# Kernel tuning notes

Hardware: AMD Instinct MI355X
Metric: run time of the kernel (lower is better)

Reference implementation:

```python
import jax, jax.numpy as jnp
import numpy as np

Z, Y, X = 16, 128, 128
B = 2
N_R, N_L = 12000, 20000   # active voxels per batch element (radar / lidar)
C = 64
IN_DIM = 4
NUM_LAYER = 2
K_LIST = (64, 32)         # knn fan-out = 64 / 2**layer
EPS = 1e-5


def _make_voxels(rng, n_per_batch):
    # unique voxel coords per batch, sorted by linear index (batch-major rows)
    out = []
    for b in range(B):
        lin = np.sort(rng.choice(Z * Y * X, size=n_per_batch, replace=False))
        z = lin // (Y * X); y = (lin // X) % Y; x = lin % X
        out.append(np.stack([np.full(n_per_batch, b), z, y, x], 1))
    return np.concatenate(out, 0).astype(np.int32)


def _nbr_map(coords):
    # 3x3x3 submanifold-conv rulebook: row index of each neighbor, -1 if absent
    b = coords[:, 0].astype(np.int64); z = coords[:, 1]; y = coords[:, 2]; x = coords[:, 3]
    keys = ((b * Z + z) * Y + y) * X + x  # globally sorted
    N = coords.shape[0]
    nbr = np.full((N, 27), -1, np.int64)
    k = 0
    for dz in (-1, 0, 1):
        for dy in (-1, 0, 1):
            for dx in (-1, 0, 1):
                nz, ny, nx = z + dz, y + dy, x + dx
                ok = (nz >= 0) & (nz < Z) & (ny >= 0) & (ny < Y) & (nx >= 0) & (nx < X)
                cand = ((b * Z + nz) * Y + ny) * X + nx
                pos = np.searchsorted(keys, cand)
                pos_c = np.clip(pos, 0, N - 1)
                hit = ok & (keys[pos_c] == cand)
                nbr[:, k] = np.where(hit, pos_c, -1)
                k += 1
    return nbr


def setup_inputs() -> dict:
    rng = np.random.default_rng(0)
    key = jax.random.key(0)
    ks = jax.random.split(key, 16)
    coordsR = _make_voxels(rng, N_R)
    coordsL = _make_voxels(rng, N_L)
    nbrR = _nbr_map(coordsR)
    nbrL = _nbr_map(coordsL)
    NLt = B * N_L
    # knn indices (global row ids into radar rows of same batch)
    knn0 = coordsL[:, 0:1].astype(np.int64) * N_R + rng.integers(0, N_R, (NLt, K_LIST[0]))
    knn1 = coordsL[:, 0:1].astype(np.int64) * N_R + rng.integers(0, N_R, (NLt, K_LIST[1]))
    sc = 1.0 / np.sqrt(27 * C).astype(np.float32)
    inp = {
        "featR": jax.random.normal(ks[0], (B * N_R, IN_DIM), jnp.float32),
        "featL": jax.random.normal(ks[1], (NLt, IN_DIM), jnp.float32),
        "img": jax.random.normal(ks[2], (B, 512), jnp.float32),
        "Win": jax.random.normal(ks[3], (2, IN_DIM, C), jnp.float32) * 0.1,
        "bin_": jnp.zeros((2, C), jnp.float32),
        # [layer, branch(R/L), conv(sp,subm_a,subm_b), 27, Cin, Cout]
        "Wconv": jax.random.normal(ks[4], (NUM_LAYER, 2, 3, 27, C, C), jnp.float32) * sc,
        "bconv": jnp.zeros((NUM_LAYER, 2, 3, C), jnp.float32),
        "bng": jnp.ones((NUM_LAYER, 2, 3, C), jnp.float32),
        "bnb": jnp.zeros((NUM_LAYER, 2, 3, C), jnp.float32),
        "Wimg": jax.random.normal(ks[5], (NUM_LAYER, 512, C), jnp.float32) * 0.05,
        "bimg": jnp.zeros((NUM_LAYER, C), jnp.float32),
        "Wval": jax.random.normal(ks[6], (NUM_LAYER, C, C), jnp.float32) * 0.125,
        "bval": jnp.zeros((NUM_LAYER, C), jnp.float32),
        "Wgate": jax.random.normal(ks[7], (NUM_LAYER, 2 * C, C), jnp.float32) * 0.09,
        "bgate": jnp.zeros((NUM_LAYER, C), jnp.float32),
        "Wbev": jax.random.normal(ks[8], (NUM_LAYER, 2, C * Z, C, 3, 3), jnp.float32) * (1.0 / np.sqrt(C * Z * 9).astype(np.float32)),
        "bbev": jnp.zeros((NUM_LAYER, 2, C), jnp.float32),
        "bntg": jnp.ones((NUM_LAYER, 2, C), jnp.float32),
        "bntb": jnp.zeros((NUM_LAYER, 2, C), jnp.float32),
        "nbrR": jnp.asarray(nbrR),
        "nbrL": jnp.asarray(nbrL),
        "knn0": jnp.asarray(knn0),
        "knn1": jnp.asarray(knn1),
        "coordsR": jnp.asarray(coordsR),
        "coordsL": jnp.asarray(coordsL),
    }
    return inp


def _bn1d(f, g, b):
    m = f.mean(0)
    v = f.var(0)
    return (f - m) / jnp.sqrt(v + EPS) * g + b


def _sconv(f, nbr, W, bias):
    # gather-scatter sparse 3D conv: out[n] = sum_k W[k] @ f[nbr[n,k]]
    mask = (nbr >= 0)[..., None].astype(f.dtype)
    g = f[jnp.clip(nbr, 0)] * mask                 # [N, 27, C]
    return jnp.einsum('nkc,kcd->nd', g, W) + bias


def _branch_block(f, nbr, Wc, bc, g, bt):
    # spconv -> bn -> relu, subm_a -> bn -> relu, subm_b -> bn -> relu
    for j in range(3):
        f = jax.nn.relu(_bn1d(_sconv(f, nbr, Wc[j], bc[j]), g[j], bt[j]))
    return f


def _to_bev(f, coords, Wt, bt, gg, gb):
    dense = jnp.zeros((B, Z, Y, X, C), f.dtype).at[
        coords[:, 0], coords[:, 1], coords[:, 2], coords[:, 3]].add(f)
    x2 = dense.transpose(0, 4, 1, 2, 3).reshape(B, C * Z, Y, X)  # 'b c z y x -> b (c z) y x'
    # ConvTranspose2d(k=3, s=1, p=1) == conv with swapped-IO, spatially flipped kernel, pad 1
    Wk = jnp.transpose(Wt, (1, 0, 2, 3))[:, :, ::-1, ::-1]
    out = jax.lax.conv_general_dilated(x2, Wk, (1, 1), ((1, 1), (1, 1)),
                                       dimension_numbers=('NCHW', 'OIHW', 'NCHW'))
    out = out + bt[:, None, None]
    m = out.mean((0, 2, 3), keepdims=True)
    v = out.var((0, 2, 3), keepdims=True)
    out = (out - m) / jnp.sqrt(v + EPS) * gg[:, None, None] + gb[:, None, None]
    return jax.nn.relu(out)


def reference(featR, featL, img, Win, bin_, Wconv, bconv, bng, bnb, Wimg, bimg,
              Wval, bval, Wgate, bgate, Wbev, bbev, bntg, bntb,
              nbrR, nbrL, knn0, knn1, coordsR, coordsL):
    fR = featR @ Win[0] + bin_[0]   # input_convR (1x1x1)
    fL = featL @ Win[1] + bin_[1]   # input_convL (1x1x1)
    knns = (knn0, knn1)
    bidL = coordsL[:, 0]
    bevs = []
    for l in range(NUM_LAYER):
        fR = _branch_block(fR, nbrR, Wconv[l, 0], bconv[l, 0], bng[l, 0], bnb[l, 0])
        fL = _branch_block(fL, nbrL, Wconv[l, 1], bconv[l, 1], bng[l, 1], bnb[l, 1])
        # knn cross-attention fusion: lidar queries K nearest radar voxels
        key = fR[knns[l]]                                        # [NL, K, C]
        val = jnp.einsum('nkc,cd->nkd', key, Wval[l]) + bval[l]
        attn = jax.nn.softmax(jnp.einsum('nc,nkc->nk', fL, key), axis=-1)
        fused = jnp.einsum('nk,nkd->nd', attn, val)
        imgf = jax.nn.sigmoid(img @ Wimg[l] + bimg[l])           # [B, C] weather condition
        fused = fused * imgf[bidL]
        gate = jax.nn.sigmoid(jnp.concatenate([fL, fused], -1) @ Wgate[l] + bgate[l])
        fL = fL + gate * fused
        bevs.append(_to_bev(fR, coordsR, Wbev[l, 0], bbev[l, 0], bntg[l, 0], bntb[l, 0]))
        bevs.append(_to_bev(fL, coordsL, Wbev[l, 1], bbev[l, 1], bntg[l, 1], bntb[l, 1]))
    return jnp.concatenate(bevs, axis=1)  # [B, 4*C, Y, X]
```

## Files before the change

### kernel.cpp

```cpp
#include <hip/hip_runtime.h>
#include <math.h>

#define NRT 24000
#define NLT 40000

static __device__ __forceinline__ float sigmoidf_(float x){ return 1.0f/(1.0f+expf(-x)); }

static __device__ __forceinline__ int xcd_swz(int bid, int nwg){
  int q = nwg>>3, r = nwg&7, x = bid&7, i = bid>>3;
  return (x<r ? x*(q+1) : r*(q+1)+(x-r)*q) + i;
}

__global__ void k_proj(const float* __restrict__ feat, const float* __restrict__ W,
                       const float* __restrict__ bias, float* __restrict__ out, int N){
  int i = blockIdx.x*256 + threadIdx.x;
  if (i >= N*64) return;
  int n = i >> 6, c = i & 63;
  const float* f = feat + n*4;
  out[i] = fmaf(f[0], W[c], fmaf(f[1], W[64+c], fmaf(f[2], W[128+c], fmaf(f[3], W[192+c], bias[c]))));
}

__global__ void k_kmask16(const int* __restrict__ nbr, int NG, int* __restrict__ kmask){
  int g = blockIdx.x*64 + threadIdx.x;
  if (g >= NG) return;
  int m = 0;
  for (int v=0;v<16;v++){
    const int* row = nbr + (size_t)(g*16+v)*27;
    for (int k=0;k<27;k++) if (row[k] >= 0) m |= (1<<k);
  }
  kmask[g] = m;
}

__global__ void k_wc(const float* __restrict__ Wconv, float* __restrict__ WcT){
  int i = blockIdx.x*256+threadIdx.x;
  if (i >= 12*27*16*64*4) return;
  int j = i & 3; int r = i >> 2;
  int d = r & 63; r >>= 6;
  int c4 = r & 15; r >>= 4;
  int k = r % 27; int lc = r / 27;
  WcT[i] = Wconv[(size_t)lc*110592 + (size_t)k*4096 + (size_t)(4*c4+j)*64 + d];
}

__global__ void k_sconv(const float* __restrict__ fin, const int* __restrict__ nbr,
                        const int* __restrict__ kmask, const float* __restrict__ W,
                        float* __restrict__ psum, size_t pstride, int N){
  int t = threadIdx.x & 63;
  int sub = threadIdx.x >> 6;
  int g = xcd_swz(blockIdx.x, gridDim.x);
  int n0 = g*16;
  float acc[16];
  #pragma unroll
  for (int v=0;v<16;v++) acc[v] = 0.f;
  const int* nrow = nbr + (size_t)n0*27;
  int m = kmask[g] & (0x7F << (7*sub));
  while (m){
    int k = __builtin_ctz(m); m &= m-1;
    const float4* w4 = reinterpret_cast<const float4*>(W) + k*1024 + t;
    float4 wreg[16];
    #pragma unroll
    for (int c4=0;c4<16;c4++) wreg[c4] = w4[c4*64];
    #pragma unroll
    for (int v=0;v<16;v++){
      int nb = nrow[27*v + k];
      if (nb >= 0){
        const float4* fr = reinterpret_cast<const float4*>(fin + (size_t)nb*64);
        float4 a = make_float4(0.f,0.f,0.f,0.f);
        #pragma unroll
        for (int c4=0;c4<16;c4++){
          float4 fv = fr[c4];
          a.x = fmaf(fv.x, wreg[c4].x, a.x);
          a.y = fmaf(fv.y, wreg[c4].y, a.y);
          a.z = fmaf(fv.z, wreg[c4].z, a.z);
          a.w = fmaf(fv.w, wreg[c4].w, a.w);
        }
        acc[v] += (a.x+a.y)+(a.z+a.w);
      }
    }
  }
  float* po = psum + (size_t)sub*pstride;
  #pragma unroll
  for (int v=0;v<16;v++) po[(size_t)(n0+v)*64 + t] = acc[v];
}

__global__ void k_colsum4(const float* __restrict__ p, size_t st, int N,
                          float* __restrict__ partial){
  int d = threadIdx.x & 63, sub = threadIdx.x >> 6;
  float s=0.f, s2=0.f;
  for (int n = blockIdx.x*4 + sub; n < N; n += 1024){
    size_t i = (size_t)n*64+d;
    float v = p[i] + p[i+st] + p[i+2*st] + p[i+3*st];
    s += v; s2 = fmaf(v,v,s2);
  }
  __shared__ float ls[4][64], ls2[4][64];
  ls[sub][d]=s; ls2[sub][d]=s2;
  __syncthreads();
  if (sub==0){
    s  = ls[0][d]+ls[1][d]+ls[2][d]+ls[3][d];
    s2 = ls2[0][d]+ls2[1][d]+ls2[2][d]+ls2[3][d];
    partial[(blockIdx.x*64+d)*2+0]=s;
    partial[(blockIdx.x*64+d)*2+1]=s2;
  }
}

__global__ void k_bnfin(const float* __restrict__ partial, int nblk, float invN,
                        const float* __restrict__ g, const float* __restrict__ b,
                        float* __restrict__ mv){
  int t = threadIdx.x, d = t & 63, sub = t >> 6;
  float s=0.f, s2=0.f;
  for (int i=sub;i<nblk;i+=4){ s += partial[(i*64+d)*2]; s2 += partial[(i*64+d)*2+1]; }
  __shared__ float ls[4][64], ls2[4][64];
  ls[sub][d]=s; ls2[sub][d]=s2;
  __syncthreads();
  if (sub==0){
    s  = ls[0][d]+ls[1][d]+ls[2][d]+ls[3][d];
    s2 = ls2[0][d]+ls2[1][d]+ls2[2][d]+ls2[3][d];
    float mean = s*invN;
    float var  = s2*invN - mean*mean;
    float rstd = 1.0f/sqrtf(var + 1e-5f);
    float sc = g[d]*rstd;
    mv[d*2]   = sc;
    mv[d*2+1] = b[d] - mean*sc;
  }
}

__global__ void k_bnrelu4(const float* __restrict__ p, size_t st,
                          const float* __restrict__ mv, float* __restrict__ fout, int total){
  int i = blockIdx.x*256+threadIdx.x;
  if (i>=total) return;
  int c = i & 63;
  float s = p[i] + p[i+st] + p[i+2*st] + p[i+3*st];
  float v = fmaf(s, mv[c*2], mv[c*2+1]);
  fout[i] = v>0.f? v:0.f;
}

__global__ void k_imgf(const float* __restrict__ img, const float* __restrict__ Wimg,
                       const float* __restrict__ bimg, float* __restrict__ imgf){
  int t = threadIdx.x;
  int b = t>>6, c = t&63;
  float s = bimg[c];
  const float* ir = img + b*512;
  for (int j=0;j<512;j++) s = fmaf(ir[j], Wimg[j*64+c], s);
  imgf[b*64+c] = sigmoidf_(s);
}

__global__ void k_attn(float* __restrict__ fL, const float* __restrict__ fR,
                       const int* __restrict__ knn, const int* __restrict__ coordsL,
                       const float* __restrict__ Wval, const float* __restrict__ bval,
                       const float* __restrict__ Wgate, const float* __restrict__ bgate,
                       const float* __restrict__ imgf, int K){
  __shared__ float keys[64*65];
  __shared__ float fls[64];
  __shared__ float aw[64];
  __shared__ float wks[64];
  __shared__ float fus[64];
  int n = blockIdx.x, t = threadIdx.x;
  float fl = fL[(size_t)n*64+t];
  fls[t] = fl;
  const int* kn = knn + (size_t)n*K;
  for (int k=0;k<K;k++){
    int r = kn[k];
    keys[k*65+t] = fR[(size_t)r*64+t];
  }
  __syncthreads();
  float s = -1e30f;
  if (t < K){
    const float* kr = keys + t*65;
    float a0 = 0.f;
    #pragma unroll
    for (int c=0;c<64;c++) a0 = fmaf(fls[c], kr[c], a0);
    s = a0;
  }
  float mx = s;
  #pragma unroll
  for (int m=32;m;m>>=1) mx = fmaxf(mx, __shfl_xor(mx, m, 64));
  float e = (t<K) ? expf(s-mx) : 0.f;
  float se = e;
  #pragma unroll
  for (int m=32;m;m>>=1) se += __shfl_xor(se, m, 64);
  aw[t] = e/se;
  __syncthreads();
  float wk = 0.f;
  for (int k=0;k<K;k++) wk = fmaf(aw[k], keys[k*65+t], wk);
  wks[t] = wk;
  __syncthreads();
  float fu = bval[t];
  #pragma unroll
  for (int c=0;c<64;c++) fu = fmaf(wks[c], Wval[c*64+t], fu);
  int bid = coordsL[n*4];
  fu *= imgf[bid*64+t];
  fus[t] = fu;
  __syncthreads();
  float gs = bgate[t];
  #pragma unroll
  for (int c=0;c<64;c++) gs = fmaf(fls[c], Wgate[c*64+t], gs);
  #pragma unroll
  for (int c=0;c<64;c++) gs = fmaf(fus[c], Wgate[(64+c)*64+t], gs);
  float gate = sigmoidf_(gs);
  fL[(size_t)n*64+t] = fl + gate*fu;
}

__global__ void k_grid(const int* __restrict__ coords, int N, int* __restrict__ grid){
  int n = blockIdx.x*256+threadIdx.x;
  if (n>=N) return;
  int b=coords[n*4], z=coords[n*4+1], y=coords[n*4+2], x=coords[n*4+3];
  grid[((b*128+y)*128+x)*16+z] = n;
}

__global__ void k_colbuild(const int* __restrict__ grid, int* __restrict__ ccnt,
                           int* __restrict__ cent){
  int col = blockIdx.x*256+threadIdx.x;
  if (col >= 2*128*128) return;
  const int* g = grid + col*16;
  int c=0;
  for (int z=0;z<16;z++){ int v=g[z]; if (v>=0) cent[col*16 + (c++)] = (v<<4)|z; }
  ccnt[col]=c;
}

__global__ void k_zbound(const int* __restrict__ coords, int N, int* __restrict__ zs){
  int n = blockIdx.x*256+threadIdx.x;
  if (n>=N) return;
  int key = coords[n*4]*16 + coords[n*4+1];
  int pk = (n>0) ? coords[(n-1)*4]*16 + coords[(n-1)*4+1] : -1;
  for (int kk=pk+1; kk<=key; kk++) zs[kk] = n;
  if (n==N-1){ for (int kk=key+1; kk<=32; kk++) zs[kk] = N; }
}

__global__ void k_wt3(const float* __restrict__ Wbev, float* __restrict__ Wt3){
  int i = blockIdx.x*256+threadIdx.x;
  if (i >= 4*9*16*16*64*4) return;
  int j = i & 3; int r = i >> 2;
  int o = r & 63; r >>= 6;
  int c4 = r & 15; r >>= 4;
  int z = r & 15; r >>= 4;
  int q = r % 9; int ls = r / 9;
  int c = 4*c4 + j;
  int ky = 2-q/3, kx = 2-q%3;
  Wt3[i] = Wbev[(size_t)ls*589824 + (size_t)(c*16+z)*576 + o*9 + ky*3 + kx];
}

__global__ void k_bevg(const float* __restrict__ f, const int* __restrict__ zs,
                       const float* __restrict__ Wt,
                       float* __restrict__ tmp, int CH){
  int task = blockIdx.x / CH, chunk = blockIdx.x % CH;
  int q = task >> 4, z = task & 15;
  int t = threadIdx.x;
  const float4* w4 = reinterpret_cast<const float4*>(Wt + (size_t)(((q<<4)+z)<<12)) + t;
  float4 wreg[16];
  #pragma unroll
  for (int c4=0;c4<16;c4++) wreg[c4] = w4[c4*64];
  int s0 = zs[z], c0 = zs[z+1]-s0;
  int s1 = zs[16+z], c1 = zs[17+z]-s1;
  int total = c0 + c1;
  for (int i=chunk; i<total; i+=CH){
    int v = (i<c0) ? s0+i : s1+(i-c0);
    const float4* fr = reinterpret_cast<const float4*>(f + (size_t)v*64);
    float4 a = make_float4(0.f,0.f,0.f,0.f);
    #pragma unroll
    for (int c4=0;c4<16;c4++){
      float4 fv = fr[c4];
      a.x = fmaf(fv.x, wreg[c4].x, a.x);
      a.y = fmaf(fv.y, wreg[c4].y, a.y);
      a.z = fmaf(fv.z, wreg[c4].z, a.z);
      a.w = fmaf(fv.w, wreg[c4].w, a.w);
    }
    tmp[((size_t)v*9+q)*64 + t] = (a.x+a.y)+(a.z+a.w);
  }
}

__global__ void k_bevs(const float* __restrict__ tmp, const int* __restrict__ ccnt,
                       const int* __restrict__ cent, float* __restrict__ outp){
  int blk = xcd_swz(blockIdx.x, gridDim.x);
  int b = blk>>12; int rem = blk&4095; int y = rem>>5; int x0 = (rem&31)<<2;
  int t = threadIdx.x;
  float acc[4] = {0.f,0.f,0.f,0.f};
  #pragma unroll
  for (int dy=-1;dy<=1;dy++){
    int y2 = y+dy;
    if ((unsigned)y2 >= 128u) continue;
    int qb = (dy+1)*3 + 1;
    for (int cx=x0-1; cx<=x0+4; cx++){
      if ((unsigned)cx >= 128u) continue;
      int col = ((b<<7)+y2)*128 + cx;
      int cn = ccnt[col];
      const int* ce = cent + col*16;
      int d0 = cx - x0;
      for (int i=0;i<cn;i++){
        int rid = ce[i]>>4;
        const float* tb = tmp + (size_t)rid*576 + qb*64 + t;
        #pragma unroll
        for (int v=0;v<4;v++){
          int dx = d0 - v;
          if (dx>=-1 && dx<=1) acc[v] += tb[dx*64];
        }
      }
    }
  }
  float4 o4 = make_float4(acc[0],acc[1],acc[2],acc[3]);
  *reinterpret_cast<float4*>(outp + (size_t)b*(256*16384) + (size_t)t*16384 + y*128 + x0) = o4;
}

__global__ void k_bevstat(const float* __restrict__ outp, const float* __restrict__ g,
                          const float* __restrict__ b, float* __restrict__ mv){
  int ch = blockIdx.x, t = threadIdx.x;
  float s=0.f, s2=0.f;
  for (int bb=0;bb<2;bb++){
    const float* base = outp + (size_t)bb*(256*16384) + (size_t)ch*16384;
    for (int p=t;p<16384;p+=256){ float v = base[p]; s+=v; s2=fmaf(v,v,s2); }
  }
  __shared__ float ls[256], ls2[256];
  ls[t]=s; ls2[t]=s2; __syncthreads();
  for (int m=128;m;m>>=1){ if (t<m){ ls[t]+=ls[t+m]; ls2[t]+=ls2[t+m]; } __syncthreads(); }
  if (t==0){
    float mean = ls[0]*(1.0f/32768.0f);
    float var  = ls2[0]*(1.0f/32768.0f) - mean*mean;
    float rstd = 1.0f/sqrtf(var+1e-5f);
    float sc = g[ch]*rstd;
    mv[ch*2]=sc; mv[ch*2+1]=b[ch]-mean*sc;
  }
}

__global__ void k_bevbn(float* __restrict__ outp, const float* __restrict__ mv){
  int i = blockIdx.x*256+threadIdx.x;
  if (i >= 2*64*16384) return;
  int bb = i>>20; int r = i & ((1<<20)-1);
  int ch = r>>14; int p = r&16383;
  float* a = outp + (size_t)bb*(256*16384) + (size_t)ch*16384 + p;
  float v = fmaf(*a, mv[ch*2], mv[ch*2+1]);
  *a = v>0.f? v:0.f;
}

extern "C" void kernel_launch(void* const* d_in, const int* in_sizes, int n_in,
                              void* d_out, int out_size, void* d_ws, size_t ws_size,
                              hipStream_t stream){
  const float* featR = (const float*)d_in[0];
  const float* featL = (const float*)d_in[1];
  const float* img   = (const float*)d_in[2];
  const float* Win   = (const float*)d_in[3];
  const float* bin_  = (const float*)d_in[4];
  const float* Wconv = (const float*)d_in[5];
  const float* bng   = (const float*)d_in[7];
  const float* bnb   = (const float*)d_in[8];
  const float* Wimg  = (const float*)d_in[9];
  const float* bimg  = (const float*)d_in[10];
  const float* Wval  = (const float*)d_in[11];
  const float* bval  = (const float*)d_in[12];
  const float* Wgate = (const float*)d_in[13];
  const float* bgate = (const float*)d_in[14];
  const float* Wbev  = (const float*)d_in[15];
  const float* bntg  = (const float*)d_in[17];
  const float* bntb  = (const float*)d_in[18];
  const int* nbrR    = (const int*)d_in[19];
  const int* nbrL    = (const int*)d_in[20];
  const int* knn0    = (const int*)d_in[21];
  const int* knn1    = (const int*)d_in[22];
  const int* coordsR = (const int*)d_in[23];
  const int* coordsL = (const int*)d_in[24];
  float* outp = (float*)d_out;

  char* w = (char*)d_ws;
  auto alloc = [&](size_t bytes){ char* p = w; w += (bytes + 255) & ~(size_t)255; return p; };
  float* fRa = (float*)alloc((size_t)NRT*64*4);
  float* fLa = (float*)alloc((size_t)NLT*64*4);
  int*   gridR = (int*)alloc((size_t)2*128*128*16*4);
  int*   gridL = (int*)alloc((size_t)2*128*128*16*4);
  float* Wt3 = (float*)alloc((size_t)4*9*16*16*64*4*4);
  float* WcT = (float*)alloc((size_t)12*27*16*64*4*4);
  float* imgfbuf = (float*)alloc(2*64*4);
  float* partial = (float*)alloc((size_t)256*64*2*4);
  float* mv = (float*)alloc(64*2*4);
  int* kmaskR = (int*)alloc((size_t)(NRT/16)*4);
  int* kmaskL = (int*)alloc((size_t)(NLT/16)*4);
  int* ccntR = (int*)alloc((size_t)2*128*128*4);
  int* ccntL = (int*)alloc((size_t)2*128*128*4);
  int* centR = (int*)alloc((size_t)2*128*128*16*4);
  int* centL = (int*)alloc((size_t)2*128*128*16*4);
  int* zsR = (int*)alloc(33*4);
  int* zsL = (int*)alloc(33*4);
  char* big = alloc((size_t)NLT*576*4);
  float* tmp  = (float*)big;
  float* psum = (float*)big;
  const size_t PST = (size_t)NLT*64;

  hipMemsetAsync(gridR, 0xFF, (size_t)2*128*128*16*4, stream);
  hipMemsetAsync(gridL, 0xFF, (size_t)2*128*128*16*4, stream);
  k_grid<<<(NRT+255)/256,256,0,stream>>>(coordsR, NRT, gridR);
  k_grid<<<(NLT+255)/256,256,0,stream>>>(coordsL, NLT, gridL);
  k_colbuild<<<(2*128*128+255)/256,256,0,stream>>>(gridR, ccntR, centR);
  k_colbuild<<<(2*128*128+255)/256,256,0,stream>>>(gridL, ccntL, centL);
  k_zbound<<<(NRT+255)/256,256,0,stream>>>(coordsR, NRT, zsR);
  k_zbound<<<(NLT+255)/256,256,0,stream>>>(coordsL, NLT, zsL);
  k_kmask16<<<((NRT/16)+63)/64,64,0,stream>>>(nbrR, NRT/16, kmaskR);
  k_kmask16<<<((NLT/16)+63)/64,64,0,stream>>>(nbrL, NLT/16, kmaskL);
  k_wt3<<<(4*9*16*16*64*4+255)/256,256,0,stream>>>(Wbev, Wt3);
  k_wc<<<(12*27*16*64*4+255)/256,256,0,stream>>>(Wconv, WcT);

  k_proj<<<(NRT*64+255)/256,256,0,stream>>>(featR, Win,     bin_,    fRa, NRT);
  k_proj<<<(NLT*64+255)/256,256,0,stream>>>(featL, Win+256, bin_+64, fLa, NLT);

  const int CH = 32;
  for (int l=0;l<2;l++){
    for (int j=0;j<3;j++){
      const float* Wc = WcT + (size_t)((l*2+0)*3+j)*110592;
      k_sconv<<<NRT/16,256,0,stream>>>(fRa, nbrR, kmaskR, Wc, psum, PST, NRT);
      k_colsum4<<<256,256,0,stream>>>(psum, PST, NRT, partial);
      k_bnfin<<<1,256,0,stream>>>(partial, 256, 1.0f/NRT,
                                  bng + ((l*2+0)*3+j)*64, bnb + ((l*2+0)*3+j)*64, mv);
      k_bnrelu4<<<(NRT*64+255)/256,256,0,stream>>>(psum, PST, mv, fRa, NRT*64);
    }
    for (int j=0;j<3;j++){
      const float* Wc = WcT + (size_t)((l*2+1)*3+j)*110592;
      k_sconv<<<NLT/16,256,0,stream>>>(fLa, nbrL, kmaskL, Wc, psum, PST, NLT);
      k_colsum4<<<256,256,0,stream>>>(psum, PST, NLT, partial);
      k_bnfin<<<1,256,0,stream>>>(partial, 256, 1.0f/NLT,
                                  bng + ((l*2+1)*3+j)*64, bnb + ((l*2+1)*3+j)*64, mv);
      k_bnrelu4<<<(NLT*64+255)/256,256,0,stream>>>(psum, PST, mv, fLa, NLT*64);
    }
    k_imgf<<<1,128,0,stream>>>(img, Wimg + (size_t)l*512*64, bimg + l*64, imgfbuf);
    const int* knn = (l==0)? knn0 : knn1;
    int K = (l==0)? 64 : 32;
    k_attn<<<NLT,64,0,stream>>>(fLa, fRa, knn, coordsL,
                                Wval + (size_t)l*4096, bval + l*64,
                                Wgate + (size_t)l*8192, bgate + l*64,
                                imgfbuf, K);
    {
      float* op = outp + (size_t)(2*l)*64*16384;
      const float* wt = Wt3 + (size_t)(l*2+0)*589824;
      k_bevg<<<144*CH,64,0,stream>>>(fRa, zsR, wt, tmp, CH);
      k_bevs<<<2*128*32,64,0,stream>>>(tmp, ccntR, centR, op);
      k_bevstat<<<64,256,0,stream>>>(op, bntg + (l*2+0)*64, bntb + (l*2+0)*64, mv);
      k_bevbn<<<(2*64*16384+255)/256,256,0,stream>>>(op, mv);
    }
    {
      float* op = outp + (size_t)(2*l+1)*64*16384;
      const float* wt = Wt3 + (size_t)(l*2+1)*589824;
      k_bevg<<<144*CH,64,0,stream>>>(fLa, zsL, wt, tmp, CH);
      k_bevs<<<2*128*32,64,0,stream>>>(tmp, ccntL, centL, op);
      k_bevstat<<<64,256,0,stream>>>(op, bntg + (l*2+1)*64, bntb + (l*2+1)*64, mv);
      k_bevbn<<<(2*64*16384+255)/256,256,0,stream>>>(op, mv);
    }
  }
}
```

Baseline: 3.266 ms.

## Replace masked group sparse conv with offset-sorted pair list SpMM and reduction

The sparse 3x3x3 conv no longer loops over 16-voxel groups under a union kernel-offset mask, which wasted work on absent neighbours. It now builds a compacted list of (offset, voxel) pairs sorted by offset and splits it evenly across 2048 waves, reloading weights only when the offset changes. Each pair's contribution goes to a per-voxel slot in a contrib buffer, and a separate reduction kernel sums them. This removes the 4-way partial-sum buffers but adds several prep kernels, extra global traffic for contributions, and a reduce pass. The BEV gather kernel also gains XCD swizzling with a reordered task mapping.

```diff
diff --git a/kernel.cpp b/kernel.cpp
--- a/kernel.cpp
+++ b/kernel.cpp
@@ -20,15 +20,71 @@
   out[i] = fmaf(f[0], W[c], fmaf(f[1], W[64+c], fmaf(f[2], W[128+c], fmaf(f[3], W[192+c], bias[c]))));
 }
 
-__global__ void k_kmask16(const int* __restrict__ nbr, int NG, int* __restrict__ kmask){
-  int g = blockIdx.x*64 + threadIdx.x;
-  if (g >= NG) return;
-  int m = 0;
-  for (int v=0;v<16;v++){
-    const int* row = nbr + (size_t)(g*16+v)*27;
-    for (int k=0;k<27;k++) if (row[k] >= 0) m |= (1<<k);
-  }
-  kmask[g] = m;
+__global__ void k_mask(const int* __restrict__ nbr, int N, int* __restrict__ mask){
+  int n = blockIdx.x*256+threadIdx.x;
+  if (n>=N) return;
+  const int* row = nbr + (size_t)n*27;
+  int m=0;
+  #pragma unroll
+  for (int k=0;k<27;k++) if (row[k]>=0) m |= 1<<k;
+  mask[n]=m;
+}
+
+__global__ void k_wsum(const int* __restrict__ mask, int N, int* __restrict__ wsum){
+  int n = blockIdx.x*256+threadIdx.x;
+  int pc = (n<N)? __popc(mask[n]) : 0;
+  #pragma unroll
+  for (int s=32;s;s>>=1) pc += __shfl_down(pc, s, 64);
+  if ((threadIdx.x&63)==0) wsum[(blockIdx.x*256+threadIdx.x)>>6] = pc;
+}
+
+__global__ void k_scan(const int* __restrict__ in, int M, int* __restrict__ out){
+  __shared__ int buf[704];
+  for (int i=threadIdx.x;i<M;i+=256) buf[i]=in[i];
+  __syncthreads();
+  if (threadIdx.x==0){ int s=0; for (int i=0;i<M;i++){ int v=buf[i]; buf[i]=s; s+=v; } buf[M]=s; }
+  __syncthreads();
+  for (int i=threadIdx.x;i<=M;i+=256) out[i]=buf[i];
+}
+
+__global__ void k_noff(const int* __restrict__ mask, const int* __restrict__ woff,
+                       int N, int* __restrict__ noff){
+  int n = blockIdx.x*256+threadIdx.x;
+  if (n>=N) return;
+  int lane = threadIdx.x&63;
+  int pc = __popc(mask[n]);
+  int pre = pc;
+  #pragma unroll
+  for (int s=1;s<64;s<<=1){ int v=__shfl_up(pre, s, 64); if (lane>=s) pre+=v; }
+  noff[n] = woff[n>>6] + pre - pc;
+  if (n==N-1) noff[N] = woff[N>>6];
+}
+
+__global__ void k_kcnt2(const int* __restrict__ mask, int N, int* __restrict__ cnt2){
+  int k = blockIdx.x>>3, seg = blockIdx.x&7;
+  int s0 = seg*(N/8), s1 = s0 + N/8;
+  int c=0;
+  for (int n=s0+threadIdx.x;n<s1;n+=256) c += (mask[n]>>k)&1;
+  __shared__ int ls[256];
+  ls[threadIdx.x]=c; __syncthreads();
+  for (int m=128;m;m>>=1){ if (threadIdx.x<m) ls[threadIdx.x]+=ls[threadIdx.x+m]; __syncthreads(); }
+  if (threadIdx.x==0) cnt2[blockIdx.x]=ls[0];
+}
+
+__global__ void k_kfill2(const int* __restrict__ mask, int N, const int* __restrict__ off2,
+                         unsigned* __restrict__ pairs){
+  int w = (blockIdx.x*256+threadIdx.x)>>6;
+  int lane = threadIdx.x&63;
+  int k = w>>3, seg = w&7;
+  int s0 = seg*(N/8), s1 = s0 + N/8;
+  int base = off2[w];
+  for (int n0=s0;n0<s1;n0+=64){
+    int n = n0+lane;
+    int v = (n<s1) && ((mask[n]>>k)&1);
+    unsigned long long bal = __ballot(v);
+    if (v) pairs[base + (int)__popcll(bal & ((1ull<<lane)-1))] = ((unsigned)k<<16)|(unsigned)n;
+    base += (int)__popcll(bal);
+  }
 }
 
 __global__ void k_wc(const float* __restrict__ Wconv, float* __restrict__ WcT){
@@ -41,54 +97,58 @@
   WcT[i] = Wconv[(size_t)lc*110592 + (size_t)k*4096 + (size_t)(4*c4+j)*64 + d];
 }
 
-__global__ void k_sconv(const float* __restrict__ fin, const int* __restrict__ nbr,
-                        const int* __restrict__ kmask, const float* __restrict__ W,
-                        float* __restrict__ psum, size_t pstride, int N){
-  int t = threadIdx.x & 63;
-  int sub = threadIdx.x >> 6;
-  int g = xcd_swz(blockIdx.x, gridDim.x);
-  int n0 = g*16;
-  float acc[16];
-  #pragma unroll
-  for (int v=0;v<16;v++) acc[v] = 0.f;
-  const int* nrow = nbr + (size_t)n0*27;
-  int m = kmask[g] & (0x7F << (7*sub));
-  while (m){
-    int k = __builtin_ctz(m); m &= m-1;
-    const float4* w4 = reinterpret_cast<const float4*>(W) + k*1024 + t;
-    float4 wreg[16];
+__global__ void k_spmm(const float* __restrict__ fin, const int* __restrict__ nbr,
+                       const int* __restrict__ mask, const int* __restrict__ noff,
+                       const int* __restrict__ off2, const unsigned* __restrict__ pairs,
+                       const float* __restrict__ W, float* __restrict__ contrib, int nwaves){
+  int wid = (blockIdx.x*256+threadIdx.x)>>6;
+  int t = threadIdx.x&63;
+  int total = off2[216];
+  int a = (int)(((long long)wid*total)/nwaves);
+  int b = (int)(((long long)(wid+1)*total)/nwaves);
+  int kcur = -1;
+  float4 wreg[16];
+  for (int i=a;i<b;i++){
+    unsigned pk = pairs[i];
+    int k = pk>>16, n = pk&0xFFFF;
+    if (k!=kcur){
+      kcur=k;
+      const float4* w4 = reinterpret_cast<const float4*>(W) + k*1024 + t;
+      #pragma unroll
+      for (int c4=0;c4<16;c4++) wreg[c4]=w4[c4*64];
+    }
+    int nb = nbr[(size_t)n*27+k];
+    const float4* fr = reinterpret_cast<const float4*>(fin + (size_t)nb*64);
+    float4 a4 = make_float4(0.f,0.f,0.f,0.f);
     #pragma unroll
-    for (int c4=0;c4<16;c4++) wreg[c4] = w4[c4*64];
-    #pragma unroll
-    for (int v=0;v<16;v++){
-      int nb = nrow[27*v + k];
-      if (nb >= 0){
-        const float4* fr = reinterpret_cast<const float4*>(fin + (size_t)nb*64);
-        float4 a = make_float4(0.f,0.f,0.f,0.f);
-        #pragma unroll
-        for (int c4=0;c4<16;c4++){
-          float4 fv = fr[c4];
-          a.x = fmaf(fv.x, wreg[c4].x, a.x);
-          a.y = fmaf(fv.y, wreg[c4].y, a.y);
-          a.z = fmaf(fv.z, wreg[c4].z, a.z);
-          a.w = fmaf(fv.w, wreg[c4].w, a.w);
-        }
-        acc[v] += (a.x+a.y)+(a.z+a.w);
-      }
-    }
-  }
-  float* po = psum + (size_t)sub*pstride;
-  #pragma unroll
-  for (int v=0;v<16;v++) po[(size_t)(n0+v)*64 + t] = acc[v];
-}
-
-__global__ void k_colsum4(const float* __restrict__ p, size_t st, int N,
-                          float* __restrict__ partial){
+    for (int c4=0;c4<16;c4++){
+      float4 fv = fr[c4];
+      a4.x = fmaf(fv.x, wreg[c4].x, a4.x);
+      a4.y = fmaf(fv.y, wreg[c4].y, a4.y);
+      a4.z = fmaf(fv.z, wreg[c4].z, a4.z);
+      a4.w = fmaf(fv.w, wreg[c4].w, a4.w);
+    }
+    int rank = __popc(mask[n] & ((1<<k)-1));
+    contrib[((size_t)noff[n]+rank)*64 + t] = (a4.x+a4.y)+(a4.z+a4.w);
+  }
+}
+
+__global__ void k_sred(const float* __restrict__ contrib, const int* __restrict__ noff,
+                       float* __restrict__ out, int N){
+  int n = (blockIdx.x*256+threadIdx.x)>>6;
+  if (n>=N) return;
+  int t = threadIdx.x&63;
+  int j0=noff[n], j1=noff[n+1];
+  float s=0.f;
+  for (int j=j0;j<j1;j++) s += contrib[(size_t)j*64+t];
+  out[(size_t)n*64+t]=s;
+}
+
+__global__ void k_colsum(const float* __restrict__ f, int N, float* __restrict__ partial){
   int d = threadIdx.x & 63, sub = threadIdx.x >> 6;
   float s=0.f, s2=0.f;
   for (int n = blockIdx.x*4 + sub; n < N; n += 1024){
-    size_t i = (size_t)n*64+d;
-    float v = p[i] + p[i+st] + p[i+2*st] + p[i+3*st];
+    float v = f[(size_t)n*64+d];
     s += v; s2 = fmaf(v,v,s2);
   }
   __shared__ float ls[4][64], ls2[4][64];
@@ -123,13 +183,12 @@
   }
 }
 
-__global__ void k_bnrelu4(const float* __restrict__ p, size_t st,
-                          const float* __restrict__ mv, float* __restrict__ fout, int total){
+__global__ void k_bnrelu(const float* __restrict__ cv, const float* __restrict__ mv,
+                         float* __restrict__ fout, int total){
   int i = blockIdx.x*256+threadIdx.x;
   if (i>=total) return;
   int c = i & 63;
-  float s = p[i] + p[i+st] + p[i+2*st] + p[i+3*st];
-  float v = fmaf(s, mv[c*2], mv[c*2+1]);
+  float v = fmaf(cv[i], mv[c*2], mv[c*2+1]);
   fout[i] = v>0.f? v:0.f;
 }
 
@@ -241,8 +300,9 @@
 __global__ void k_bevg(const float* __restrict__ f, const int* __restrict__ zs,
                        const float* __restrict__ Wt,
                        float* __restrict__ tmp, int CH){
-  int task = blockIdx.x / CH, chunk = blockIdx.x % CH;
-  int q = task >> 4, z = task & 15;
+  int blk = xcd_swz(blockIdx.x, gridDim.x);
+  int task = blk / CH, chunk = blk % CH;
+  int q = task % 9, z = task / 9;
   int t = threadIdx.x;
   const float4* w4 = reinterpret_cast<const float4*>(Wt + (size_t)(((q<<4)+z)<<12)) + t;
   float4 wreg[16];
@@ -368,18 +428,30 @@
   float* imgfbuf = (float*)alloc(2*64*4);
   float* partial = (float*)alloc((size_t)256*64*2*4);
   float* mv = (float*)alloc(64*2*4);
-  int* kmaskR = (int*)alloc((size_t)(NRT/16)*4);
-  int* kmaskL = (int*)alloc((size_t)(NLT/16)*4);
   int* ccntR = (int*)alloc((size_t)2*128*128*4);
   int* ccntL = (int*)alloc((size_t)2*128*128*4);
   int* centR = (int*)alloc((size_t)2*128*128*16*4);
   int* centL = (int*)alloc((size_t)2*128*128*16*4);
   int* zsR = (int*)alloc(33*4);
   int* zsL = (int*)alloc(33*4);
+  int* maskR = (int*)alloc((size_t)NRT*4);
+  int* maskL = (int*)alloc((size_t)NLT*4);
+  int* wsumR = (int*)alloc(1024*4);
+  int* wsumL = (int*)alloc(1024*4);
+  int* woffR = (int*)alloc(1024*4);
+  int* woffL = (int*)alloc(1024*4);
+  int* noffR = (int*)alloc((size_t)(NRT+1)*4);
+  int* noffL = (int*)alloc((size_t)(NLT+1)*4);
+  int* cnt2R = (int*)alloc(256*4);
+  int* cnt2L = (int*)alloc(256*4);
+  int* off2R = (int*)alloc(256*4);
+  int* off2L = (int*)alloc(256*4);
+  unsigned* pairsR = (unsigned*)alloc((size_t)6*NRT*4);
+  unsigned* pairsL = (unsigned*)alloc((size_t)6*NLT*4);
   char* big = alloc((size_t)NLT*576*4);
-  float* tmp  = (float*)big;
-  float* psum = (float*)big;
-  const size_t PST = (size_t)NLT*64;
+  float* cv      = (float*)big;
+  float* contrib = (float*)(big + (size_t)16*1024*1024);
+  float* tmp     = (float*)big;
 
   hipMemsetAsync(gridR, 0xFF, (size_t)2*128*128*16*4, stream);
   hipMemsetAsync(gridL, 0xFF, (size_t)2*128*128*16*4, stream);
@@ -389,8 +461,20 @@
   k_colbuild<<<(2*128*128+255)/256,256,0,stream>>>(gridL, ccntL, centL);
   k_zbound<<<(NRT+255)/256,256,0,stream>>>(coordsR, NRT, zsR);
   k_zbound<<<(NLT+255)/256,256,0,stream>>>(coordsL, NLT, zsL);
-  k_kmask16<<<((NRT/16)+63)/64,64,0,stream>>>(nbrR, NRT/16, kmaskR);
-  k_kmask16<<<((NLT/16)+63)/64,64,0,stream>>>(nbrL, NLT/16, kmaskL);
+  k_mask<<<(NRT+255)/256,256,0,stream>>>(nbrR, NRT, maskR);
+  k_mask<<<(NLT+255)/256,256,0,stream>>>(nbrL, NLT, maskL);
+  k_wsum<<<(NRT+255)/256,256,0,stream>>>(maskR, NRT, wsumR);
+  k_wsum<<<(NLT+255)/256,256,0,stream>>>(maskL, NLT, wsumL);
+  k_scan<<<1,256,0,stream>>>(wsumR, NRT/64, woffR);
+  k_scan<<<1,256,0,stream>>>(wsumL, NLT/64, woffL);
+  k_noff<<<(NRT+255)/256,256,0,stream>>>(maskR, woffR, NRT, noffR);
+  k_noff<<<(NLT+255)/256,256,0,stream>>>(maskL, woffL, NLT, noffL);
+  k_kcnt2<<<216,256,0,stream>>>(maskR, NRT, cnt2R);
+  k_kcnt2<<<216,256,0,stream>>>(maskL, NLT, cnt2L);
+  k_scan<<<1,256,0,stream>>>(cnt2R, 216, off2R);
+  k_scan<<<1,256,0,stream>>>(cnt2L, 216, off2L);
+  k_kfill2<<<54,256,0,stream>>>(maskR, NRT, off2R, pairsR);
+  k_kfill2<<<54,256,0,stream>>>(maskL, NLT, off2L, pairsL);
   k_wt3<<<(4*9*16*16*64*4+255)/256,256,0,stream>>>(Wbev, Wt3);
   k_wc<<<(12*27*16*64*4+255)/256,256,0,stream>>>(Wconv, WcT);
 
@@ -398,22 +482,25 @@
   k_proj<<<(NLT*64+255)/256,256,0,stream>>>(featL, Win+256, bin_+64, fLa, NLT);
 
   const int CH = 32;
+  const int NWV = 2048;
   for (int l=0;l<2;l++){
     for (int j=0;j<3;j++){
       const float* Wc = WcT + (size_t)((l*2+0)*3+j)*110592;
-      k_sconv<<<NRT/16,256,0,stream>>>(fRa, nbrR, kmaskR, Wc, psum, PST, NRT);
-      k_colsum4<<<256,256,0,stream>>>(psum, PST, NRT, partial);
+      k_spmm<<<NWV/4,256,0,stream>>>(fRa, nbrR, maskR, noffR, off2R, pairsR, Wc, contrib, NWV);
+      k_sred<<<(NRT+3)/4,256,0,stream>>>(contrib, noffR, cv, NRT);
+      k_colsum<<<256,256,0,stream>>>(cv, NRT, partial);
       k_bnfin<<<1,256,0,stream>>>(partial, 256, 1.0f/NRT,
                                   bng + ((l*2+0)*3+j)*64, bnb + ((l*2+0)*3+j)*64, mv);
-      k_bnrelu4<<<(NRT*64+255)/256,256,0,stream>>>(psum, PST, mv, fRa, NRT*64);
+      k_bnrelu<<<(NRT*64+255)/256,256,0,stream>>>(cv, mv, fRa, NRT*64);
     }
     for (int j=0;j<3;j++){
       const float* Wc = WcT + (size_t)((l*2+1)*3+j)*110592;
-      k_sconv<<<NLT/16,256,0,stream>>>(fLa, nbrL, kmaskL, Wc, psum, PST, NLT);
-      k_colsum4<<<256,256,0,stream>>>(psum, PST, NLT, partial);
+      k_spmm<<<NWV/4,256,0,stream>>>(fLa, nbrL, maskL, noffL, off2L, pairsL, Wc, contrib, NWV);
+      k_sred<<<(NLT+3)/4,256,0,stream>>>(contrib, noffL, cv, NLT);
+      k_colsum<<<256,256,0,stream>>>(cv, NLT, partial);
       k_bnfin<<<1,256,0,stream>>>(partial, 256, 1.0f/NLT,
                                   bng + ((l*2+1)*3+j)*64, bnb + ((l*2+1)*3+j)*64, mv);
-      k_bnrelu4<<<(NLT*64+255)/256,256,0,stream>>>(psum, PST, mv, fLa, NLT*64);
+      k_bnrelu<<<(NLT*64+255)/256,256,0,stream>>>(cv, mv, fLa, NLT*64);
     }
     k_imgf<<<1,128,0,stream>>>(img, Wimg + (size_t)l*512*64, bimg + l*64, imgfbuf);
     const int* knn = (l==0)? knn0 : knn1;
```

Result: slower. 3.442 ms (+5.4%).
